# Optimization experiments

Measured on AMD Instinct MI355X. Metric: run time of the kernel, lower is better.

## Reference

```python
import jax, jax.numpy as jnp
import numpy as np

DIM = 1024
HEADS = 16
NEG = 1.0e10


def split_heads(v, heads):
    # Faithful to source: reshape puts heads LAST, then transpose -> [b, h, s, hd]
    b, s, d = v.shape
    hd = d // heads
    v = v.reshape(b, s, hd, heads)
    return jnp.transpose(v, (0, 3, 1, 2))


def merge_heads(v):
    b, h, s, hd = v.shape
    v = jnp.transpose(v, (0, 2, 3, 1))  # [b, s, hd, h]
    return v.reshape(b, s, h * hd)


def setup_inputs() -> dict:
    key = jax.random.key(0)
    kx, kq, kk, kv, ko = jax.random.split(key, 5)
    x = jax.random.normal(kx, (2, 2048, DIM), dtype=jnp.float32)
    # RandomNormal initializer default stddev 0.05
    qw = 0.05 * jax.random.normal(kq, (DIM, DIM), dtype=jnp.float32)
    kw = 0.05 * jax.random.normal(kk, (DIM, DIM), dtype=jnp.float32)
    vw = 0.05 * jax.random.normal(kv, (DIM, DIM), dtype=jnp.float32)
    ow = 0.05 * jax.random.normal(ko, (DIM, DIM), dtype=jnp.float32)
    return {"x": x, "qw": qw, "kw": kw, "vw": vw, "ow": ow}


def reference(x, qw, kw, vw, ow):
    b, s, d = x.shape
    Q = split_heads(x @ qw, HEADS)  # [b, h, s, hd]
    K = split_heads(x @ kw, HEADS)
    V = split_heads(x @ vw, HEADS)
    # NOTE: source scales by sqrt(dim), not sqrt(head_dim)
    score = jnp.einsum('bhqd,bhkd->bhqk', Q, K) / jnp.sqrt(jnp.float32(d))
    causal = jnp.tril(jnp.ones((1, 1, s, s), dtype=score.dtype))
    score = score - NEG * (1.0 - causal)
    weights = jax.nn.softmax(score, axis=-1)
    attn = jnp.einsum('bhqk,bhkd->bhqd', weights, V)
    return merge_heads(attn) @ ow
```

## Files before the change

### kernel.cpp

```cpp
#include <hip/hip_runtime.h>
#include <stdint.h>

typedef unsigned short ushort_t;
typedef __bf16 bf16x8 __attribute__((ext_vector_type(8)));
typedef float f32x4 __attribute__((ext_vector_type(4)));

#define DIM 1024
#define HEADS 16
#define HD 64
#define BATCH 2
#define SEQ 2048
#define MTOT (BATCH*SEQ)

#define C2F 0.045084220027780106f

__device__ __forceinline__ ushort_t f2bf(float f) {
    uint32_t u = __float_as_uint(f);
    uint32_t r = (u + 0x7FFFu + ((u >> 16) & 1u)) >> 16;
    return (ushort_t)r;
}

__device__ __forceinline__ uint32_t pack2bf(float a, float b) {
    return ((uint32_t)f2bf(b) << 16) | (uint32_t)f2bf(a);
}

__device__ __forceinline__ f32x4 mfma16(bf16x8 a, bf16x8 b, f32x4 c) {
    return __builtin_amdgcn_mfma_f32_16x16x32_bf16(a, b, c, 0, 0, 0);
}

__device__ __forceinline__ void glds16(const ushort_t* g, ushort_t* l) {
    __builtin_amdgcn_global_load_lds(
        (const __attribute__((address_space(1))) unsigned int*)g,
        (__attribute__((address_space(3))) unsigned int*)l, 16, 0, 0);
}

__global__ void k_conv_x(const float* __restrict__ x, ushort_t* __restrict__ xb, int n4) {
    int i = blockIdx.x * blockDim.x + threadIdx.x;
    if (i < n4) {
        const float4 v = ((const float4*)x)[i];
        ushort4 o;
        o.x = f2bf(v.x); o.y = f2bf(v.y); o.z = f2bf(v.z); o.w = f2bf(v.w);
        ((ushort4*)xb)[i] = o;
    }
}

__global__ void k_transpose_w(const float* __restrict__ w0, const float* __restrict__ w1,
                              const float* __restrict__ w2, const float* __restrict__ w3,
                              ushort_t* __restrict__ wt) {
    __shared__ float t[32][33];
    const int z = blockIdx.z;
    const float* w = (z == 0) ? w0 : (z == 1) ? w1 : (z == 2) ? w2 : w3;
    ushort_t* o = wt + (size_t)z * DIM * DIM;
    int n0 = blockIdx.x * 32;
    int k0 = blockIdx.y * 32;
    int tx = threadIdx.x, ty = threadIdx.y;
    if (z < 3) {
#pragma unroll
        for (int i = 0; i < 4; i++)
            t[ty + i * 8][tx] = w[(size_t)(k0 + ty + i * 8) * DIM + n0 + tx];
        __syncthreads();
#pragma unroll
        for (int i = 0; i < 4; i++) {
            int n = n0 + ty + i * 8;
            int np = (n & 15) * 64 + (n >> 4);
            o[(size_t)np * DIM + k0 + tx] = f2bf(t[tx][ty + i * 8]);
        }
    } else {
#pragma unroll
        for (int i = 0; i < 4; i++) {
            int kp = k0 + ty + i * 8;
            int k = (kp & 63) * 16 + (kp >> 6);
            t[ty + i * 8][tx] = w[(size_t)k * DIM + n0 + tx];
        }
        __syncthreads();
#pragma unroll
        for (int i = 0; i < 4; i++)
            o[(size_t)(n0 + ty + i * 8) * DIM + k0 + tx] = f2bf(t[tx][ty + i * 8]);
    }
}

__global__ __launch_bounds__(256) void k_qkv(const ushort_t* __restrict__ xb,
                                             const ushort_t* __restrict__ wt,
                                             ushort_t* __restrict__ qp,
                                             ushort_t* __restrict__ kp,
                                             ushort_t* __restrict__ vp) {
    __shared__ __align__(16) ushort_t lA[128 * 32];
    __shared__ __align__(16) ushort_t lB[128 * 32];
    const int z = blockIdx.z;
    const ushort_t* w = wt + (size_t)z * DIM * DIM;
    ushort_t* dst = (z == 0) ? qp : (z == 1) ? kp : vp;
    const float sc = (z == 0) ? C2F : 1.0f;
    const int tid = threadIdx.x;
    const int wave = tid >> 6;
    const int lane = tid & 63;
    const int l16 = lane & 15;
    const int quad = lane >> 4;
    const int m0 = blockIdx.x * 128;
    const int n0 = blockIdx.y * 128;
    const int mw = (wave & 1) * 64, nw = (wave >> 1) * 64;

    const f32x4 zero4 = {0.f, 0.f, 0.f, 0.f};
    f32x4 acc[4][4];
#pragma unroll
    for (int i = 0; i < 4; i++)
#pragma unroll
        for (int j = 0; j < 4; j++) acc[i][j] = zero4;

    const int swz = (l16 >> 1) & 3;
    for (int k0 = 0; k0 < DIM; k0 += 32) {
        __syncthreads();
#pragma unroll
        for (int j = 0; j < 2; j++) {
            int base = wave * 128 + j * 64;
            int L = base + lane;
            int row = L >> 2, cd = L & 3;
            int cs = cd ^ ((row >> 1) & 3);
            glds16(xb + (size_t)(m0 + row) * DIM + k0 + cs * 8, lA + base * 8);
            glds16(w + (size_t)(n0 + row) * DIM + k0 + cs * 8, lB + base * 8);
        }
        __syncthreads();
        bf16x8 a[4], b[4];
#pragma unroll
        for (int i = 0; i < 4; i++) {
            int rowa = mw + i * 16 + l16;
            int rowb = nw + i * 16 + l16;
            int ch = quad ^ swz;
            a[i] = *(const bf16x8*)(lA + rowa * 32 + ch * 8);
            b[i] = *(const bf16x8*)(lB + rowb * 32 + ch * 8);
        }
#pragma unroll
        for (int ni = 0; ni < 4; ni++)
#pragma unroll
            for (int mi = 0; mi < 4; mi++)
                acc[ni][mi] = mfma16(b[ni], a[mi], acc[ni][mi]);
    }

#pragma unroll
    for (int ni = 0; ni < 4; ni++)
#pragma unroll
        for (int mi = 0; mi < 4; mi++) {
            int nbase = n0 + nw + ni * 16 + quad * 4;
            int m = m0 + mw + mi * 16 + l16;
            ushort4 o;
            o.x = f2bf(acc[ni][mi][0] * sc);
            o.y = f2bf(acc[ni][mi][1] * sc);
            o.z = f2bf(acc[ni][mi][2] * sc);
            o.w = f2bf(acc[ni][mi][3] * sc);
            *(ushort4*)(dst + (size_t)m * DIM + nbase) = o;
        }
}

__global__ void k_vt(const ushort_t* __restrict__ vp, ushort_t* __restrict__ vt) {
    __shared__ ushort_t t[32][34];
    const int bh = blockIdx.z, b = bh >> 4, h = bh & 15;
    const int s0 = blockIdx.x * 32;
    const int i0 = blockIdx.y * 32;
    int tx = threadIdx.x, ty = threadIdx.y;
#pragma unroll
    for (int j = 0; j < 4; j++)
        t[ty + j * 8][tx] = vp[(size_t)(b * SEQ + s0 + ty + j * 8) * DIM + h * HD + i0 + tx];
    __syncthreads();
#pragma unroll
    for (int j = 0; j < 4; j++)
        vt[((size_t)bh * HD + i0 + ty + j * 8) * SEQ + s0 + tx] = t[tx][ty + j * 8];
}

__global__ __launch_bounds__(256) void k_attn(const ushort_t* __restrict__ qp,
                                              const ushort_t* __restrict__ kp,
                                              const ushort_t* __restrict__ vt,
                                              ushort_t* __restrict__ mg) {
    __shared__ __align__(16) ushort_t lK[2][64 * 64];
    __shared__ __align__(16) ushort_t lV[2][64 * 64];
    __shared__ __align__(16) ushort_t lP[4][16 * 72];
    const int tid = threadIdx.x;
    const int w = tid >> 6;
    const int lane = tid & 63;
    const int l16 = lane & 15;
    const int quad = lane >> 4;
    const int bh = blockIdx.y, b = bh >> 4, h = bh & 15;

    const ushort_t* Q = qp + (size_t)b * SEQ * DIM + h * HD;
    const ushort_t* K = kp + (size_t)b * SEQ * DIM + h * HD;
    const ushort_t* V = vt + (size_t)bh * HD * SEQ;

    const int swz = l16 & 7;
    ushort_t* pw = lP[w] + l16 * 72;

#pragma unroll 1
    for (int phase = 0; phase < 2; phase++) {
        const int qi = phase ? (31 - (int)blockIdx.x) : (int)blockIdx.x;
        const int qb = qi * 64;
        const int mb = qb + w * 16;
        const int nt = qi + 1;

        bf16x8 qf[2];
#pragma unroll
        for (int hf = 0; hf < 2; hf++)
            qf[hf] = *(const bf16x8*)(Q + (size_t)(mb + l16) * DIM + hf * 32 + quad * 8);

        const f32x4 zero4 = {0.f, 0.f, 0.f, 0.f};
        f32x4 oT[4];
#pragma unroll
        for (int nb = 0; nb < 4; nb++) oT[nb] = zero4;
        float lsum = 0.f;

        __syncthreads();
#pragma unroll
        for (int j = 0; j < 2; j++) {
            int base = w * 128 + j * 64;
            int L = base + lane;
            int row = L >> 3, cd = L & 7;
            int cs = cd ^ (row & 7);
            glds16(K + (size_t)row * DIM + cs * 8, lK[0] + base * 8);
            glds16(V + (size_t)row * SEQ + cs * 8, lV[0] + base * 8);
        }

        int cur = 0;
        for (int kt = 0; kt < nt; kt++) {
            const int kb = kt * 64;
            __syncthreads();
            if (kt + 1 < nt) {
                const int kb2 = kb + 64;
#pragma unroll
                for (int j = 0; j < 2; j++) {
                    int base = w * 128 + j * 64;
                    int L = base + lane;
                    int row = L >> 3, cd = L & 7;
                    int cs = cd ^ (row & 7);
                    glds16(K + (size_t)(kb2 + row) * DIM + cs * 8, lK[cur ^ 1] + base * 8);
                    glds16(V + (size_t)row * SEQ + kb2 + cs * 8, lV[cur ^ 1] + base * 8);
                }
            }

            bf16x8 kf[4][2], vf[4][2];
#pragma unroll
            for (int c = 0; c < 4; c++)
#pragma unroll
                for (int hf = 0; hf < 2; hf++) {
                    int row = c * 16 + l16;
                    int ch = (hf * 4 + quad) ^ swz;
                    kf[c][hf] = *(const bf16x8*)(lK[cur] + row * 64 + ch * 8);
                }
#pragma unroll
            for (int nb = 0; nb < 4; nb++)
#pragma unroll
                for (int pr = 0; pr < 2; pr++) {
                    int row = nb * 16 + l16;
                    int ch = (pr * 4 + quad) ^ swz;
                    vf[nb][pr] = *(const bf16x8*)(lV[cur] + row * 64 + ch * 8);
                }

            f32x4 s4[4];
#pragma unroll
            for (int c = 0; c < 4; c++) {
                f32x4 t = zero4;
                t = mfma16(kf[c][0], qf[0], t);
                t = mfma16(kf[c][1], qf[1], t);
                s4[c] = t;
            }

            const bool needmask = (kt == nt - 1);
            const int qrow = mb + l16;
            float p[4][4];
#pragma unroll
            for (int c = 0; c < 4; c++)
#pragma unroll
                for (int r = 0; r < 4; r++) {
                    float e = exp2f(s4[c][r]);
                    if (needmask && (kb + c * 16 + quad * 4 + r) > qrow) e = 0.f;
                    p[c][r] = e;
                    lsum += e;
                }

#pragma unroll
            for (int c = 0; c < 4; c++) {
                *(uint32_t*)(pw + c * 16 + quad * 4) = pack2bf(p[c][0], p[c][1]);
                *(uint32_t*)(pw + c * 16 + quad * 4 + 2) = pack2bf(p[c][2], p[c][3]);
            }
            bf16x8 pa[2];
#pragma unroll
            for (int pr = 0; pr < 2; pr++)
                pa[pr] = *(const bf16x8*)(pw + pr * 32 + quad * 8);

#pragma unroll
            for (int nb = 0; nb < 4; nb++) {
                oT[nb] = mfma16(vf[nb][0], pa[0], oT[nb]);
                oT[nb] = mfma16(vf[nb][1], pa[1], oT[nb]);
            }
            cur ^= 1;
        }

        lsum += __shfl_xor(lsum, 16);
        lsum += __shfl_xor(lsum, 32);
        float inv = 1.0f / lsum;
        int srow = mb + l16;
#pragma unroll
        for (int nb = 0; nb < 4; nb++) {
            ushort4 o;
            o.x = f2bf(oT[nb][0] * inv);
            o.y = f2bf(oT[nb][1] * inv);
            o.z = f2bf(oT[nb][2] * inv);
            o.w = f2bf(oT[nb][3] * inv);
            *(ushort4*)(mg + ((size_t)b * SEQ + srow) * DIM + h * HD + nb * 16 + quad * 4) = o;
        }
    }
}

__global__ __launch_bounds__(256) void k_out(const ushort_t* __restrict__ a_in,
                                             const ushort_t* __restrict__ wt,
                                             float* __restrict__ out) {
    __shared__ __align__(16) ushort_t lA[128 * 32];
    __shared__ __align__(16) ushort_t lB[128 * 32];
    const int tid = threadIdx.x;
    const int wave = tid >> 6;
    const int lane = tid & 63;
    const int l16 = lane & 15;
    const int quad = lane >> 4;
    const int m0 = blockIdx.x * 128;
    const int n0 = blockIdx.y * 128;
    const int mw = (wave & 1) * 64, nw = (wave >> 1) * 64;

    const f32x4 zero4 = {0.f, 0.f, 0.f, 0.f};
    f32x4 acc[4][4];
#pragma unroll
    for (int i = 0; i < 4; i++)
#pragma unroll
        for (int j = 0; j < 4; j++) acc[i][j] = zero4;

    const int swz = (l16 >> 1) & 3;
    for (int k0 = 0; k0 < DIM; k0 += 32) {
        __syncthreads();
#pragma unroll
        for (int j = 0; j < 2; j++) {
            int base = wave * 128 + j * 64;
            int L = base + lane;
            int row = L >> 2, cd = L & 3;
            int cs = cd ^ ((row >> 1) & 3);
            glds16(a_in + (size_t)(m0 + row) * DIM + k0 + cs * 8, lA + base * 8);
            glds16(wt + (size_t)(n0 + row) * DIM + k0 + cs * 8, lB + base * 8);
        }
        __syncthreads();
        bf16x8 a[4], b[4];
#pragma unroll
        for (int i = 0; i < 4; i++) {
            int rowa = mw + i * 16 + l16;
            int rowb = nw + i * 16 + l16;
            int ch = quad ^ swz;
            a[i] = *(const bf16x8*)(lA + rowa * 32 + ch * 8);
            b[i] = *(const bf16x8*)(lB + rowb * 32 + ch * 8);
        }
#pragma unroll
        for (int ni = 0; ni < 4; ni++)
#pragma unroll
            for (int mi = 0; mi < 4; mi++)
                acc[ni][mi] = mfma16(b[ni], a[mi], acc[ni][mi]);
    }

#pragma unroll
    for (int ni = 0; ni < 4; ni++)
#pragma unroll
        for (int mi = 0; mi < 4; mi++) {
            int nbase = n0 + nw + ni * 16 + quad * 4;
            int m = m0 + mw + mi * 16 + l16;
            *(float4*)(out + (size_t)m * DIM + nbase) = *(float4*)&acc[ni][mi];
        }
}

extern "C" void kernel_launch(void* const* d_in, const int* in_sizes, int n_in,
                              void* d_out, int out_size, void* d_ws, size_t ws_size,
                              hipStream_t stream) {
    const float* x  = (const float*)d_in[0];
    const float* qw = (const float*)d_in[1];
    const float* kw = (const float*)d_in[2];
    const float* vw = (const float*)d_in[3];
    const float* ow = (const float*)d_in[4];
    float* out = (float*)d_out;

    ushort_t* xb = (ushort_t*)d_ws;
    ushort_t* wt = xb + (size_t)MTOT * DIM;
    ushort_t* qp = wt + (size_t)4 * DIM * DIM;
    ushort_t* kp = qp + (size_t)MTOT * DIM;
    ushort_t* vp = kp + (size_t)MTOT * DIM;
    ushort_t* vt = vp + (size_t)MTOT * DIM;
    ushort_t* mg = xb;

    k_conv_x<<<dim3(MTOT * DIM / 4 / 256), dim3(256), 0, stream>>>(x, xb, MTOT * DIM / 4);
    k_transpose_w<<<dim3(32, 32, 4), dim3(32, 8), 0, stream>>>(qw, kw, vw, ow, wt);
    k_qkv<<<dim3(MTOT / 128, DIM / 128, 3), dim3(256), 0, stream>>>(xb, wt, qp, kp, vp);
    k_vt<<<dim3(SEQ / 32, HD / 32, BATCH * HEADS), dim3(32, 8), 0, stream>>>(vp, vt);
    k_attn<<<dim3(SEQ / 128, BATCH * HEADS), dim3(256), 0, stream>>>(qp, kp, vt, mg);
    k_out<<<dim3(MTOT / 128, DIM / 128), dim3(256), 0, stream>>>(mg, wt + (size_t)3 * DIM * DIM, out);
}
```

Before: 197.7 us.

## Merge prep kernels, deepen GEMM K-tile, compute softmax sums via MFMA

Merges the x conversion and weight transpose into one launch so the separate conversion launch goes away. Doubles the K step of the QKV and output GEMMs from 32 to 64, with a wider XOR swizzle, so each k-tile needs half as many barriers. In attention, the row sums are now accumulated with an MFMA against a ones vector, which replaces per-element adds and cross-lane shuffles. Probabilities are packed to bf16 with a byte-permute that truncates instead of rounding. That truncation adds some numerical error, and the larger tiles double LDS use in the GEMMs, which could lower occupancy.

```diff
diff --git a/kernel.cpp b/kernel.cpp
--- a/kernel.cpp
+++ b/kernel.cpp
@@ -20,8 +20,8 @@
     return (ushort_t)r;
 }
 
-__device__ __forceinline__ uint32_t pack2bf(float a, float b) {
-    return ((uint32_t)f2bf(b) << 16) | (uint32_t)f2bf(a);
+__device__ __forceinline__ uint32_t permpack(float lo, float hi) {
+    return __builtin_amdgcn_perm(__float_as_uint(hi), __float_as_uint(lo), 0x07060302u);
 }
 
 __device__ __forceinline__ f32x4 mfma16(bf16x8 a, bf16x8 b, f32x4 c) {
@@ -34,26 +34,30 @@
         (__attribute__((address_space(3))) unsigned int*)l, 16, 0, 0);
 }
 
-__global__ void k_conv_x(const float* __restrict__ x, ushort_t* __restrict__ xb, int n4) {
-    int i = blockIdx.x * blockDim.x + threadIdx.x;
-    if (i < n4) {
-        const float4 v = ((const float4*)x)[i];
-        ushort4 o;
-        o.x = f2bf(v.x); o.y = f2bf(v.y); o.z = f2bf(v.z); o.w = f2bf(v.w);
-        ((ushort4*)xb)[i] = o;
+__global__ void k_prep(const float* __restrict__ x,
+                       const float* __restrict__ w0, const float* __restrict__ w1,
+                       const float* __restrict__ w2, const float* __restrict__ w3,
+                       ushort_t* __restrict__ wt, ushort_t* __restrict__ xb) {
+    const int z = blockIdx.z;
+    int tx = threadIdx.x, ty = threadIdx.y;
+    if (z == 4) {
+        int bid = blockIdx.y * 32 + blockIdx.x;
+        int t = ty * 32 + tx;
+#pragma unroll
+        for (int u = 0; u < 4; u++) {
+            int i = bid * 1024 + u * 256 + t;
+            const float4 v = ((const float4*)x)[i];
+            ushort4 o;
+            o.x = f2bf(v.x); o.y = f2bf(v.y); o.z = f2bf(v.z); o.w = f2bf(v.w);
+            ((ushort4*)xb)[i] = o;
+        }
+        return;
     }
-}
-
-__global__ void k_transpose_w(const float* __restrict__ w0, const float* __restrict__ w1,
-                              const float* __restrict__ w2, const float* __restrict__ w3,
-                              ushort_t* __restrict__ wt) {
     __shared__ float t[32][33];
-    const int z = blockIdx.z;
     const float* w = (z == 0) ? w0 : (z == 1) ? w1 : (z == 2) ? w2 : w3;
     ushort_t* o = wt + (size_t)z * DIM * DIM;
     int n0 = blockIdx.x * 32;
     int k0 = blockIdx.y * 32;
-    int tx = threadIdx.x, ty = threadIdx.y;
     if (z < 3) {
 #pragma unroll
         for (int i = 0; i < 4; i++)
@@ -84,8 +88,8 @@
                                              ushort_t* __restrict__ qp,
                                              ushort_t* __restrict__ kp,
                                              ushort_t* __restrict__ vp) {
-    __shared__ __align__(16) ushort_t lA[128 * 32];
-    __shared__ __align__(16) ushort_t lB[128 * 32];
+    __shared__ __align__(16) ushort_t lA[128 * 64];
+    __shared__ __align__(16) ushort_t lB[128 * 64];
     const int z = blockIdx.z;
     const ushort_t* w = wt + (size_t)z * DIM * DIM;
     ushort_t* dst = (z == 0) ? qp : (z == 1) ? kp : vp;
@@ -106,33 +110,36 @@
 #pragma unroll
         for (int j = 0; j < 4; j++) acc[i][j] = zero4;
 
-    const int swz = (l16 >> 1) & 3;
-    for (int k0 = 0; k0 < DIM; k0 += 32) {
-        __syncthreads();
-#pragma unroll
-        for (int j = 0; j < 2; j++) {
-            int base = wave * 128 + j * 64;
+    const int swz = l16 & 7;
+    for (int k0 = 0; k0 < DIM; k0 += 64) {
+        __syncthreads();
+#pragma unroll
+        for (int j = 0; j < 4; j++) {
+            int base = wave * 256 + j * 64;
             int L = base + lane;
-            int row = L >> 2, cd = L & 3;
-            int cs = cd ^ ((row >> 1) & 3);
+            int row = L >> 3, cd = L & 7;
+            int cs = cd ^ (row & 7);
             glds16(xb + (size_t)(m0 + row) * DIM + k0 + cs * 8, lA + base * 8);
             glds16(w + (size_t)(n0 + row) * DIM + k0 + cs * 8, lB + base * 8);
         }
         __syncthreads();
-        bf16x8 a[4], b[4];
-#pragma unroll
-        for (int i = 0; i < 4; i++) {
-            int rowa = mw + i * 16 + l16;
-            int rowb = nw + i * 16 + l16;
-            int ch = quad ^ swz;
-            a[i] = *(const bf16x8*)(lA + rowa * 32 + ch * 8);
-            b[i] = *(const bf16x8*)(lB + rowb * 32 + ch * 8);
-        }
-#pragma unroll
-        for (int ni = 0; ni < 4; ni++)
-#pragma unroll
-            for (int mi = 0; mi < 4; mi++)
-                acc[ni][mi] = mfma16(b[ni], a[mi], acc[ni][mi]);
+#pragma unroll
+        for (int kk = 0; kk < 2; kk++) {
+            bf16x8 a[4], b[4];
+#pragma unroll
+            for (int i = 0; i < 4; i++) {
+                int rowa = mw + i * 16 + l16;
+                int rowb = nw + i * 16 + l16;
+                int ch = (kk * 4 + quad) ^ swz;
+                a[i] = *(const bf16x8*)(lA + rowa * 64 + ch * 8);
+                b[i] = *(const bf16x8*)(lB + rowb * 64 + ch * 8);
+            }
+#pragma unroll
+            for (int ni = 0; ni < 4; ni++)
+#pragma unroll
+                for (int mi = 0; mi < 4; mi++)
+                    acc[ni][mi] = mfma16(b[ni], a[mi], acc[ni][mi]);
+        }
     }
 
 #pragma unroll
@@ -186,6 +193,10 @@
     const int swz = l16 & 7;
     ushort_t* pw = lP[w] + l16 * 72;
 
+    union { ushort_t u[8]; bf16x8 v; } one8;
+#pragma unroll
+    for (int j = 0; j < 8; j++) one8.u[j] = 0x3F80;
+
 #pragma unroll 1
     for (int phase = 0; phase < 2; phase++) {
         const int qi = phase ? (31 - (int)blockIdx.x) : (int)blockIdx.x;
@@ -202,7 +213,7 @@
         f32x4 oT[4];
 #pragma unroll
         for (int nb = 0; nb < 4; nb++) oT[nb] = zero4;
-        float lsum = 0.f;
+        f32x4 ls = zero4;
 
         __syncthreads();
 #pragma unroll
@@ -261,21 +272,21 @@
 
             const bool needmask = (kt == nt - 1);
             const int qrow = mb + l16;
-            float p[4][4];
-#pragma unroll
-            for (int c = 0; c < 4; c++)
-#pragma unroll
-                for (int r = 0; r < 4; r++) {
-                    float e = exp2f(s4[c][r]);
-                    if (needmask && (kb + c * 16 + quad * 4 + r) > qrow) e = 0.f;
-                    p[c][r] = e;
-                    lsum += e;
+#pragma unroll
+            for (int c = 0; c < 4; c++) {
+                float e0 = exp2f(s4[c][0]);
+                float e1 = exp2f(s4[c][1]);
+                float e2 = exp2f(s4[c][2]);
+                float e3 = exp2f(s4[c][3]);
+                if (needmask) {
+                    int k = kb + c * 16 + quad * 4;
+                    if (k + 0 > qrow) e0 = 0.f;
+                    if (k + 1 > qrow) e1 = 0.f;
+                    if (k + 2 > qrow) e2 = 0.f;
+                    if (k + 3 > qrow) e3 = 0.f;
                 }
-
-#pragma unroll
-            for (int c = 0; c < 4; c++) {
-                *(uint32_t*)(pw + c * 16 + quad * 4) = pack2bf(p[c][0], p[c][1]);
-                *(uint32_t*)(pw + c * 16 + quad * 4 + 2) = pack2bf(p[c][2], p[c][3]);
+                *(uint32_t*)(pw + c * 16 + quad * 4) = permpack(e0, e1);
+                *(uint32_t*)(pw + c * 16 + quad * 4 + 2) = permpack(e2, e3);
             }
             bf16x8 pa[2];
 #pragma unroll
@@ -287,12 +298,12 @@
                 oT[nb] = mfma16(vf[nb][0], pa[0], oT[nb]);
                 oT[nb] = mfma16(vf[nb][1], pa[1], oT[nb]);
             }
+            ls = mfma16(one8.v, pa[0], ls);
+            ls = mfma16(one8.v, pa[1], ls);
             cur ^= 1;
         }
 
-        lsum += __shfl_xor(lsum, 16);
-        lsum += __shfl_xor(lsum, 32);
-        float inv = 1.0f / lsum;
+        float inv = 1.0f / ls[0];
         int srow = mb + l16;
 #pragma unroll
         for (int nb = 0; nb < 4; nb++) {
@@ -309,8 +320,8 @@
 __global__ __launch_bounds__(256) void k_out(const ushort_t* __restrict__ a_in,
                                              const ushort_t* __restrict__ wt,
                                              float* __restrict__ out) {
-    __shared__ __align__(16) ushort_t lA[128 * 32];
-    __shared__ __align__(16) ushort_t lB[128 * 32];
+    __shared__ __align__(16) ushort_t lA[128 * 64];
+    __shared__ __align__(16) ushort_t lB[128 * 64];
     const int tid = threadIdx.x;
     const int wave = tid >> 6;
     const int lane = tid & 63;
@@ -327,33 +338,36 @@
 #pragma unroll
         for (int j = 0; j < 4; j++) acc[i][j] = zero4;
 
-    const int swz = (l16 >> 1) & 3;
-    for (int k0 = 0; k0 < DIM; k0 += 32) {
-        __syncthreads();
-#pragma unroll
-        for (int j = 0; j < 2; j++) {
-            int base = wave * 128 + j * 64;
+    const int swz = l16 & 7;
+    for (int k0 = 0; k0 < DIM; k0 += 64) {
+        __syncthreads();
+#pragma unroll
+        for (int j = 0; j < 4; j++) {
+            int base = wave * 256 + j * 64;
             int L = base + lane;
-            int row = L >> 2, cd = L & 3;
-            int cs = cd ^ ((row >> 1) & 3);
+            int row = L >> 3, cd = L & 7;
+            int cs = cd ^ (row & 7);
             glds16(a_in + (size_t)(m0 + row) * DIM + k0 + cs * 8, lA + base * 8);
             glds16(wt + (size_t)(n0 + row) * DIM + k0 + cs * 8, lB + base * 8);
         }
         __syncthreads();
-        bf16x8 a[4], b[4];
-#pragma unroll
-        for (int i = 0; i < 4; i++) {
-            int rowa = mw + i * 16 + l16;
-            int rowb = nw + i * 16 + l16;
-            int ch = quad ^ swz;
-            a[i] = *(const bf16x8*)(lA + rowa * 32 + ch * 8);
-            b[i] = *(const bf16x8*)(lB + rowb * 32 + ch * 8);
-        }
-#pragma unroll
-        for (int ni = 0; ni < 4; ni++)
-#pragma unroll
-            for (int mi = 0; mi < 4; mi++)
-                acc[ni][mi] = mfma16(b[ni], a[mi], acc[ni][mi]);
+#pragma unroll
+        for (int kk = 0; kk < 2; kk++) {
+            bf16x8 a[4], b[4];
+#pragma unroll
+            for (int i = 0; i < 4; i++) {
+                int rowa = mw + i * 16 + l16;
+                int rowb = nw + i * 16 + l16;
+                int ch = (kk * 4 + quad) ^ swz;
+                a[i] = *(const bf16x8*)(lA + rowa * 64 + ch * 8);
+                b[i] = *(const bf16x8*)(lB + rowb * 64 + ch * 8);
+            }
+#pragma unroll
+            for (int ni = 0; ni < 4; ni++)
+#pragma unroll
+                for (int mi = 0; mi < 4; mi++)
+                    acc[ni][mi] = mfma16(b[ni], a[mi], acc[ni][mi]);
+        }
     }
 
 #pragma unroll
@@ -384,8 +398,7 @@
     ushort_t* vt = vp + (size_t)MTOT * DIM;
     ushort_t* mg = xb;
 
-    k_conv_x<<<dim3(MTOT * DIM / 4 / 256), dim3(256), 0, stream>>>(x, xb, MTOT * DIM / 4);
-    k_transpose_w<<<dim3(32, 32, 4), dim3(32, 8), 0, stream>>>(qw, kw, vw, ow, wt);
+    k_prep<<<dim3(32, 32, 5), dim3(32, 8), 0, stream>>>(x, qw, kw, vw, ow, wt, xb);
     k_qkv<<<dim3(MTOT / 128, DIM / 128, 3), dim3(256), 0, stream>>>(xb, wt, qp, kp, vp);
     k_vt<<<dim3(SEQ / 32, HD / 32, BATCH * HEADS), dim3(32, 8), 0, stream>>>(vp, vt);
     k_attn<<<dim3(SEQ / 128, BATCH * HEADS), dim3(256), 0, stream>>>(qp, kp, vt, mg);
```

New measurement: 188.2 us. 4.8% less time.
